# Optimization experiments

Hardware: AMD Instinct MI355X
Metric: run time of the kernel (lower is better)

## Reference

```python
import jax, jax.numpy as jnp
import numpy as np

V, E, H, L, T, B = 50257, 1024, 16, 12, 128, 16
FF = 4 * E
STD = 0.02


def setup_inputs() -> dict:
    key = jax.random.key(0)
    ks = jax.random.split(key, 20)
    n = lambda k, shape: (jax.random.normal(k, shape, dtype=jnp.float32) * STD)
    inp = {
        'idx': jax.random.randint(ks[0], (B, T), 0, V, dtype=jnp.int64),
        'targets': jax.random.randint(ks[1], (B, T), 0, V, dtype=jnp.int64),
        'tok_emb': n(ks[2], (V, E)),
        'pos_emb': n(ks[3], (T, E)),
        'wq': n(ks[4], (L, E, E)),
        'wk': n(ks[5], (L, E, E)),
        'wv': n(ks[6], (L, E, E)),
        'w_proj': n(ks[7], (L, E, E)),
        'b_proj': jnp.zeros((L, E), jnp.float32),
        'ln1_g': jnp.ones((L, E), jnp.float32),
        'ln1_b': jnp.zeros((L, E), jnp.float32),
        'ln2_g': jnp.ones((L, E), jnp.float32),
        'ln2_b': jnp.zeros((L, E), jnp.float32),
        'w_fc1': n(ks[8], (L, E, FF)),
        'b_fc1': jnp.zeros((L, FF), jnp.float32),
        'w_fc2': n(ks[9], (L, FF, E)),
        'b_fc2': jnp.zeros((L, E), jnp.float32),
        'lnf_g': jnp.ones((E,), jnp.float32),
        'lnf_b': jnp.zeros((E,), jnp.float32),
        'w_head': n(ks[10], (E, V)),
        'b_head': jnp.zeros((V,), jnp.float32),
    }
    return inp


def _layernorm(x, g, b, eps=1e-5):
    m = x.mean(-1, keepdims=True)
    v = ((x - m) ** 2).mean(-1, keepdims=True)
    return (x - m) / jnp.sqrt(v + eps) * g + b


def _forward(idx, targets, tok_emb, pos_emb, wq, wk, wv, w_proj, b_proj,
             ln1_g, ln1_b, ln2_g, ln2_b, w_fc1, b_fc1, w_fc2, b_fc2,
             lnf_g, lnf_b, w_head, b_head):
    Bb, Tt = idx.shape
    x = tok_emb[idx] + pos_emb[:Tt]  # (B, T, E)
    causal = jnp.tril(jnp.ones((Tt, Tt), dtype=bool))
    scale = E ** (-0.5)  # NOTE: original scales by full n_embd, not head_size

    def block(x, p):
        (wq_l, wk_l, wv_l, wp_l, bp_l, g1, b1, g2, b2, wf1, bf1, wf2, bf2) = p
        h = _layernorm(x, g1, b1)
        q = (h @ wq_l).reshape(Bb, Tt, H, -1)
        k = (h @ wk_l).reshape(Bb, Tt, H, -1)
        v = (h @ wv_l).reshape(Bb, Tt, H, -1)
        sc = jnp.einsum('bthd,bshd->bhts', q, k) * scale
        sc = jnp.where(causal, sc, -jnp.inf)
        att = jax.nn.softmax(sc, axis=-1)
        o = jnp.einsum('bhts,bshd->bthd', att, v).reshape(Bb, Tt, E)
        x = x + o @ wp_l + bp_l
        h2 = _layernorm(x, g2, b2)
        x = x + jax.nn.relu(h2 @ wf1 + bf1) @ wf2 + bf2
        return x, None

    x, _ = jax.lax.scan(block, x, (wq, wk, wv, w_proj, b_proj, ln1_g, ln1_b,
                                   ln2_g, ln2_b, w_fc1, b_fc1, w_fc2, b_fc2))
    x = _layernorm(x, lnf_g, lnf_b)
    logits = x @ w_head + b_head  # (B, T, V)
    logp = jax.nn.log_softmax(logits, axis=-1)
    nll = -jnp.take_along_axis(logp.reshape(Bb * Tt, -1),
                               targets.reshape(-1, 1), axis=1)
    loss = nll.mean()
    return logits, loss


def reference(idx, targets, tok_emb, pos_emb, wq, wk, wv, w_proj, b_proj,
              ln1_g, ln1_b, ln2_g, ln2_b, w_fc1, b_fc1, w_fc2, b_fc2,
              lnf_g, lnf_b, w_head, b_head):
    return _forward(idx, targets, tok_emb, pos_emb, wq, wk, wv, w_proj, b_proj,
                    ln1_g, ln1_b, ln2_g, ln2_b, w_fc1, b_fc1, w_fc2, b_fc2,
                    lnf_g, lnf_b, w_head, b_head)
```

## Files before the change

kernel.cpp:

```cpp
#include <hip/hip_runtime.h>
#include <math.h>

typedef unsigned short u16;
typedef float f32x4 __attribute__((ext_vector_type(4)));
typedef short bf16x8 __attribute__((ext_vector_type(8)));
typedef unsigned short us4 __attribute__((ext_vector_type(4)));

#define DEVI __device__ __forceinline__

DEVI float bf2f(u16 u) { return __uint_as_float(((unsigned int)u) << 16); }
DEVI u16 f2bf(float f) {
    unsigned int u = __float_as_uint(f);
    u += 0x7fffu + ((u >> 16) & 1u);
    return (u16)(u >> 16);
}

__global__ __launch_bounds__(256) void k_embed(const int* __restrict__ idx,
                                               const float* __restrict__ te,
                                               const float* __restrict__ pe,
                                               float* __restrict__ x) {
    int m = blockIdx.x;
    int t = m & 127;
    int tok = idx[m];
    const f32x4* a = (const f32x4*)(te + (long)tok * 1024);
    const f32x4* p = (const f32x4*)(pe + (long)t * 1024);
    f32x4* o = (f32x4*)(x + (long)m * 1024);
    o[threadIdx.x] = a[threadIdx.x] + p[threadIdx.x];
}

__global__ __launch_bounds__(256) void k_ln(const float* __restrict__ x,
                                            const float* __restrict__ g,
                                            const float* __restrict__ b,
                                            u16* __restrict__ out) {
    __shared__ float red[8];
    int tid = threadIdx.x, lane = tid & 63, wid = tid >> 6;
    int r = blockIdx.x;
    f32x4 v = ((const f32x4*)(x + (long)r * 1024))[tid];
    float s = v.x + v.y + v.z + v.w;
#pragma unroll
    for (int o2 = 32; o2; o2 >>= 1) s += __shfl_xor(s, o2);
    if (lane == 0) red[wid] = s;
    __syncthreads();
    float mean = (red[0] + red[1] + red[2] + red[3]) * (1.0f / 1024.0f);
    f32x4 d; d.x = v.x - mean; d.y = v.y - mean; d.z = v.z - mean; d.w = v.w - mean;
    float sq = d.x * d.x + d.y * d.y + d.z * d.z + d.w * d.w;
#pragma unroll
    for (int o2 = 32; o2; o2 >>= 1) sq += __shfl_xor(sq, o2);
    if (lane == 0) red[4 + wid] = sq;
    __syncthreads();
    float rstd = rsqrtf((red[4] + red[5] + red[6] + red[7]) * (1.0f / 1024.0f) + 1e-5f);
    f32x4 gg = ((const f32x4*)g)[tid];
    f32x4 bb = ((const f32x4*)b)[tid];
    us4 o4;
    o4.x = f2bf(d.x * rstd * gg.x + bb.x);
    o4.y = f2bf(d.y * rstd * gg.y + bb.y);
    o4.z = f2bf(d.z * rstd * gg.z + bb.z);
    o4.w = f2bf(d.w * rstd * gg.w + bb.w);
    ((us4*)(out + (long)r * 1024))[tid] = o4;
}

DEVI void tr_tile(const float* __restrict__ in, u16* __restrict__ out,
                  int K, int N, int k0, int n0, int tid, float (*tile)[65]) {
    int trow = tid >> 4;
    int tcol = (tid & 15) * 4;
#pragma unroll
    for (int p = 0; p < 4; ++p) {
        int k = k0 + trow + p * 16;
        const float* src = in + (long)k * N + n0 + tcol;
#pragma unroll
        for (int j = 0; j < 4; ++j) {
            int n = n0 + tcol + j;
            tile[trow + p * 16][tcol + j] = (n < N) ? src[j] : 0.0f;
        }
    }
    __syncthreads();
#pragma unroll
    for (int p = 0; p < 4; ++p) {
        int n = n0 + trow + p * 16;
        if (n < N) {
            us4 o4;
#pragma unroll
            for (int j = 0; j < 4; ++j) o4[j] = f2bf(tile[tcol + j][trow + p * 16]);
            *(us4*)(out + (long)n * K + k0 + tcol) = o4;
        }
    }
}

__global__ __launch_bounds__(256) void k_tr_one(const float* __restrict__ in,
                                                u16* __restrict__ out, int K, int N) {
    __shared__ float tile[64][65];
    tr_tile(in, out, K, N, blockIdx.y * 64, blockIdx.x * 64, threadIdx.x, tile);
}

__global__ __launch_bounds__(256) void k_tr_layer(
    const float* __restrict__ wq, const float* __restrict__ wk,
    const float* __restrict__ wv, const float* __restrict__ wp,
    const float* __restrict__ f1, const float* __restrict__ f2,
    u16* __restrict__ oqkv, u16* __restrict__ oproj,
    u16* __restrict__ of1, u16* __restrict__ of2) {
    __shared__ float tile[64][65];
    int id = blockIdx.x;
    const float* in; u16* out; int K, N, txx, tyy;
    if (id < 1024) {
        int t = id >> 8, s2 = id & 255;
        txx = s2 & 15; tyy = s2 >> 4; K = 1024; N = 1024;
        in = (t == 0) ? wq : (t == 1) ? wk : (t == 2) ? wv : wp;
        out = (t == 3) ? oproj : oqkv + (long)t * 1024 * 1024;
    } else if (id < 2048) {
        int s2 = id - 1024;
        txx = s2 & 63; tyy = s2 >> 6; K = 1024; N = 4096; in = f1; out = of1;
    } else {
        int s2 = id - 2048;
        txx = s2 & 15; tyy = s2 >> 4; K = 4096; N = 1024; in = f2; out = of2;
    }
    tr_tile(in, out, K, N, tyy * 64, txx * 64, threadIdx.x, tile);
}

template <int ROWS>
DEVI void stage_tile(const u16* __restrict__ g, long row0, long rowmax, int ld,
                     int col0, char* lds, int tid) {
    constexpr int NCH = ROWS * 8;
#pragma unroll
    for (int p = 0; p < NCH / 256; ++p) {
        int c = tid + p * 256;
        int row = c >> 3;
        int gslot = c & 7;
        int gdata = gslot ^ (row & 7);
        long gr = row0 + row;
        if (gr > rowmax) gr = rowmax;
        const u16* src = g + gr * (long)ld + col0 + gdata * 8;
        char* dst = lds + ((long)((tid & 192) + p * 256)) * 16;
        __builtin_amdgcn_global_load_lds(
            (const __attribute__((address_space(1))) void*)src,
            (__attribute__((address_space(3))) void*)dst, 16, 0, 0);
    }
}

template <int BN, bool OUT_BF16, bool RELU, bool HAS_BIAS, bool HAS_RES, bool GS, bool LP>
__global__ __launch_bounds__(256, 2) void k_gemm(
    const u16* __restrict__ A, const u16* __restrict__ Bt,
    const float* __restrict__ bias, const float* __restrict__ res,
    float* __restrict__ Cf, u16* __restrict__ Cb,
    int M, int N, int K, int ldc, float2* __restrict__ part, int ncb) {
    constexpr int NR = BN / 32;
    constexpr int ASZ = 128 * 64 * 2;
    constexpr int BSZ = BN * 64 * 2;
    __shared__ __align__(16) char lds[2 * (ASZ + BSZ)];
    int tid = threadIdx.x, lane = tid & 63, wid = tid >> 6;
    int l15 = lane & 15, l4 = lane >> 4;
    int wr = wid >> 1, wc = wid & 1;
    int bm = GS ? blockIdx.x : blockIdx.y;
    int bn = GS ? blockIdx.y : blockIdx.x;
    long m0 = (long)bm * 128;
    long n0 = (long)bn * BN;
    f32x4 acc[4][NR] = {};
    const int nk = K >> 6;

    stage_tile<128>(A, m0, (long)M - 1, K, 0, lds, tid);
    stage_tile<BN>(Bt, n0, (long)N - 1, K, 0, lds + ASZ, tid);
    int cur = 0;
    for (int kt = 0; kt < nk; ++kt) {
        __syncthreads();
        if (kt + 1 < nk) {
            char* nb = lds + (cur ^ 1) * (ASZ + BSZ);
            stage_tile<128>(A, m0, (long)M - 1, K, (kt + 1) << 6, nb, tid);
            stage_tile<BN>(Bt, n0, (long)N - 1, K, (kt + 1) << 6, nb + ASZ, tid);
        }
        const char* ab = lds + cur * (ASZ + BSZ);
        const char* bb = ab + ASZ;
#pragma unroll
        for (int kh = 0; kh < 2; ++kh) {
            bf16x8 af[4], bfv[NR];
#pragma unroll
            for (int mi = 0; mi < 4; ++mi) {
                int row = wr * 64 + mi * 16 + l15;
                int slot = (kh * 4 + l4) ^ (row & 7);
                af[mi] = *(const bf16x8*)(ab + (row * 8 + slot) * 16);
            }
#pragma unroll
            for (int ni = 0; ni < NR; ++ni) {
                int row = wc * (BN / 2) + ni * 16 + l15;
                int slot = (kh * 4 + l4) ^ (row & 7);
                bfv[ni] = *(const bf16x8*)(bb + (row * 8 + slot) * 16);
            }
#pragma unroll
            for (int mi = 0; mi < 4; ++mi)
#pragma unroll
                for (int ni = 0; ni < NR; ++ni)
                    acc[mi][ni] = __builtin_amdgcn_mfma_f32_16x16x32_bf16(
                        af[mi], bfv[ni], acc[mi][ni], 0, 0, 0);
        }
        cur ^= 1;
    }
    if constexpr (LP) {
        __shared__ float pmx[2][128], psm[2][128];
        float bvv[NR];
#pragma unroll
        for (int ni = 0; ni < NR; ++ni) {
            long n = n0 + wc * (BN / 2) + ni * 16 + l15;
            bvv[ni] = (HAS_BIAS && n < N) ? bias[n] : 0.0f;
        }
#pragma unroll
        for (int mi = 0; mi < 4; ++mi) {
#pragma unroll
            for (int j = 0; j < 4; ++j) {
                long m = m0 + wr * 64 + mi * 16 + l4 * 4 + j;
                float vv[NR];
                float mx = -INFINITY;
#pragma unroll
                for (int ni = 0; ni < NR; ++ni) {
                    long n = n0 + wc * (BN / 2) + ni * 16 + l15;
                    float v = acc[mi][ni][j] + bvv[ni];
                    if (n < N) Cf[m * (long)ldc + n] = v;
                    else v = -INFINITY;
                    vv[ni] = v;
                    mx = fmaxf(mx, v);
                }
#pragma unroll
                for (int ofs = 1; ofs < 16; ofs <<= 1) mx = fmaxf(mx, __shfl_xor(mx, ofs));
                float sm = 0.f;
#pragma unroll
                for (int ni = 0; ni < NR; ++ni) sm += __expf(vv[ni] - mx);
#pragma unroll
                for (int ofs = 1; ofs < 16; ofs <<= 1) sm += __shfl_xor(sm, ofs);
                if (l15 == 0) {
                    int r2 = wr * 64 + mi * 16 + l4 * 4 + j;
                    pmx[wc][r2] = mx;
                    psm[wc][r2] = sm;
                }
            }
        }
        __syncthreads();
        if (tid < 128) {
            float m1 = pmx[0][tid], m2 = pmx[1][tid];
            float nm = fmaxf(m1, m2);
            float S = psm[0][tid] * __expf(m1 - nm) + psm[1][tid] * __expf(m2 - nm);
            part[(m0 + tid) * (long)ncb + bn] = make_float2(nm, S);
        }
    } else {
#pragma unroll
        for (int ni = 0; ni < NR; ++ni) {
            long n = n0 + wc * (BN / 2) + ni * 16 + l15;
            if (n < N) {
                float bv = HAS_BIAS ? bias[n] : 0.0f;
#pragma unroll
                for (int mi = 0; mi < 4; ++mi) {
#pragma unroll
                    for (int j = 0; j < 4; ++j) {
                        long m = m0 + wr * 64 + mi * 16 + l4 * 4 + j;
                        float v = acc[mi][ni][j] + bv;
                        if (HAS_RES) v += res[m * (long)ldc + n];
                        if (RELU) v = fmaxf(v, 0.0f);
                        if (OUT_BF16) Cb[m * (long)ldc + n] = f2bf(v);
                        else Cf[m * (long)ldc + n] = v;
                    }
                }
            }
        }
    }
}

__global__ __launch_bounds__(256) void k_attn_mfma(const u16* __restrict__ qkv,
                                                   u16* __restrict__ o) {
    __shared__ __align__(16) u16 Ks[128 * 64];
    __shared__ __align__(16) u16 Vt[64 * 128];
    __shared__ __align__(16) u16 Ps[4][32 * 128];
    int tid = threadIdx.x, lane = tid & 63, w = tid >> 6;
    int l15 = lane & 15, l4 = lane >> 4;
    int b = blockIdx.x >> 4, h = blockIdx.x & 15;
    const u16* base = qkv + (long)b * 128 * 3072 + h * 64;

    stage_tile<128>(base + 1024, 0, 127, 3072, 0, (char*)Ks, tid);

    {
        const u16* vg = base + 2048;
#pragma unroll
        for (int p = 0; p < 4; ++p) {
            int s0 = (w * 4 + p) * 8;
            u16 tmp[8];
#pragma unroll
            for (int j = 0; j < 8; ++j) tmp[j] = vg[(long)(s0 + j) * 3072 + lane];
            int slot = (s0 >> 3) ^ (lane & 7);
            *(bf16x8*)((char*)Vt + lane * 256 + slot * 16) = *(bf16x8*)tmp;
        }
    }
    bf16x8 aq[2][2];
#pragma unroll
    for (int mj = 0; mj < 2; ++mj)
#pragma unroll
        for (int kk = 0; kk < 2; ++kk)
            aq[mj][kk] = *(const bf16x8*)(base + (long)(w * 32 + mj * 16 + l15) * 3072 + kk * 32 + l4 * 8);
    __syncthreads();

    f32x4 sacc[2][8] = {};
#pragma unroll
    for (int sj = 0; sj < 8; ++sj) {
        bf16x8 bk[2];
#pragma unroll
        for (int kk = 0; kk < 2; ++kk) {
            int row = sj * 16 + l15;
            int slot = (kk * 4 + l4) ^ (row & 7);
            bk[kk] = *(const bf16x8*)((char*)Ks + (row * 8 + slot) * 16);
        }
#pragma unroll
        for (int mj = 0; mj < 2; ++mj) {
            sacc[mj][sj] = __builtin_amdgcn_mfma_f32_16x16x32_bf16(aq[mj][0], bk[0], sacc[mj][sj], 0, 0, 0);
            sacc[mj][sj] = __builtin_amdgcn_mfma_f32_16x16x32_bf16(aq[mj][1], bk[1], sacc[mj][sj], 0, 0, 0);
        }
    }
    const float scale = 0.03125f;
#pragma unroll
    for (int mj = 0; mj < 2; ++mj) {
#pragma unroll
        for (int j = 0; j < 4; ++j) {
            int tq = w * 32 + mj * 16 + l4 * 4 + j;
            float mx = -INFINITY;
#pragma unroll
            for (int sj = 0; sj < 8; ++sj) {
                int s = sj * 16 + l15;
                float v = (s <= tq) ? sacc[mj][sj][j] * scale : -INFINITY;
                sacc[mj][sj][j] = v;
                mx = fmaxf(mx, v);
            }
#pragma unroll
            for (int ofs = 1; ofs < 16; ofs <<= 1) mx = fmaxf(mx, __shfl_xor(mx, ofs));
            float sm = 0.f;
#pragma unroll
            for (int sj = 0; sj < 8; ++sj) {
                float e = __expf(sacc[mj][sj][j] - mx);
                sacc[mj][sj][j] = e;
                sm += e;
            }
#pragma unroll
            for (int ofs = 1; ofs < 16; ofs <<= 1) sm += __shfl_xor(sm, ofs);
            float inv = 1.0f / sm;
            int m2 = mj * 16 + l4 * 4 + j;
            u16* prow = Ps[w] + m2 * 128;
#pragma unroll
            for (int sj = 0; sj < 8; ++sj) {
                int s = sj * 16 + l15;
                int slot = (s >> 3) ^ (m2 & 7);
                prow[slot * 8 + (s & 7)] = f2bf(sacc[mj][sj][j] * inv);
            }
        }
    }
    f32x4 oacc[2][4] = {};
#pragma unroll
    for (int kk = 0; kk < 4; ++kk) {
        bf16x8 pa[2], bv[4];
#pragma unroll
        for (int mj = 0; mj < 2; ++mj) {
            int m2 = mj * 16 + l15;
            int slot = (kk * 4 + l4) ^ (m2 & 7);
            pa[mj] = *(const bf16x8*)((char*)(Ps[w]) + m2 * 256 + slot * 16);
        }
#pragma unroll
        for (int nb = 0; nb < 4; ++nb) {
            int d = nb * 16 + l15;
            int slot = (kk * 4 + l4) ^ (d & 7);
            bv[nb] = *(const bf16x8*)((char*)Vt + d * 256 + slot * 16);
        }
#pragma unroll
        for (int mj = 0; mj < 2; ++mj)
#pragma unroll
            for (int nb = 0; nb < 4; ++nb)
                oacc[mj][nb] = __builtin_amdgcn_mfma_f32_16x16x32_bf16(pa[mj], bv[nb], oacc[mj][nb], 0, 0, 0);
    }
#pragma unroll
    for (int mj = 0; mj < 2; ++mj)
#pragma unroll
        for (int nb = 0; nb < 4; ++nb) {
            int d = nb * 16 + l15;
#pragma unroll
            for (int j = 0; j < 4; ++j) {
                int tq = w * 32 + mj * 16 + l4 * 4 + j;
                o[((long)b * 128 + tq) * 1024 + h * 64 + d] = f2bf(oacc[mj][nb][j]);
            }
        }
}

__global__ __launch_bounds__(64) void k_loss_rows2(const float2* __restrict__ part,
                                                   const float* __restrict__ logits,
                                                   const int* __restrict__ tgt,
                                                   float* __restrict__ rowloss, int ncb) {
    int r = blockIdx.x, lane = threadIdx.x;
    float M = -INFINITY, S = 0.f;
    for (int cb = lane; cb < ncb; cb += 64) {
        float2 p = part[(long)r * ncb + cb];
        float nm = fmaxf(M, p.x);
        S = S * __expf(M - nm) + p.y * __expf(p.x - nm);
        M = nm;
    }
#pragma unroll
    for (int ofs = 32; ofs; ofs >>= 1) {
        float M2 = __shfl_xor(M, ofs), S2 = __shfl_xor(S, ofs);
        float nm = fmaxf(M, M2);
        S = S * __expf(M - nm) + S2 * __expf(M2 - nm);
        M = nm;
    }
    if (lane == 0)
        rowloss[r] = (M + logf(S)) - logits[(long)r * 50257 + tgt[r]];
}

__global__ __launch_bounds__(256) void k_loss_reduce(const float* __restrict__ rowloss,
                                                     float* __restrict__ out) {
    __shared__ float red[4];
    int tid = threadIdx.x, lane = tid & 63, wid = tid >> 6;
    float s = 0.f;
    for (int i = tid; i < 2048; i += 256) s += rowloss[i];
#pragma unroll
    for (int ofs = 32; ofs; ofs >>= 1) s += __shfl_xor(s, ofs);
    if (lane == 0) red[wid] = s;
    __syncthreads();
    if (tid == 0) out[0] = (red[0] + red[1] + red[2] + red[3]) * (1.0f / 2048.0f);
}

extern "C" void kernel_launch(void* const* d_in, const int* in_sizes, int n_in,
                              void* d_out, int out_size, void* d_ws, size_t ws_size,
                              hipStream_t stream) {
    (void)in_sizes; (void)n_in; (void)out_size; (void)ws_size;
    const int*   idx     = (const int*)d_in[0];
    const int*   targets = (const int*)d_in[1];
    const float* tok_emb = (const float*)d_in[2];
    const float* pos_emb = (const float*)d_in[3];
    const float* wq      = (const float*)d_in[4];
    const float* wk      = (const float*)d_in[5];
    const float* wv      = (const float*)d_in[6];
    const float* w_proj  = (const float*)d_in[7];
    const float* b_proj  = (const float*)d_in[8];
    const float* ln1_g   = (const float*)d_in[9];
    const float* ln1_b   = (const float*)d_in[10];
    const float* ln2_g   = (const float*)d_in[11];
    const float* ln2_b   = (const float*)d_in[12];
    const float* w_fc1   = (const float*)d_in[13];
    const float* b_fc1   = (const float*)d_in[14];
    const float* w_fc2   = (const float*)d_in[15];
    const float* b_fc2   = (const float*)d_in[16];
    const float* lnf_g   = (const float*)d_in[17];
    const float* lnf_b   = (const float*)d_in[18];
    const float* w_head  = (const float*)d_in[19];
    const float* b_head  = (const float*)d_in[20];
    float* out = (float*)d_out;

    char* w = (char*)d_ws;
    auto alloc = [&](size_t bytes) {
        char* p = w;
        w += (bytes + 255) & ~(size_t)255;
        return p;
    };
    u16*    wT_qkv  = (u16*)alloc(3072L * 1024 * 2);
    u16*    wT_proj = (u16*)alloc(1024L * 1024 * 2);
    u16*    wT_f1   = (u16*)alloc(4096L * 1024 * 2);
    u16*    wT_f2   = (u16*)alloc(1024L * 4096 * 2);
    u16*    wT_head = (u16*)alloc(50257L * 1024 * 2);
    float*  x       = (float*)alloc(2048L * 1024 * 4);
    u16*    h_bf    = (u16*)alloc(2048L * 1024 * 2);
    u16*    qkvb    = (u16*)alloc(2048L * 3072 * 2);
    u16*    o_bf    = (u16*)alloc(2048L * 1024 * 2);
    u16*    ff_bf   = (u16*)alloc(2048L * 4096 * 2);
    float2* part    = (float2*)alloc(2048L * 393 * 8);
    float*  rowloss = (float*)alloc(2048L * 4);

    k_embed<<<2048, 256, 0, stream>>>(idx, tok_emb, pos_emb, x);
    k_tr_one<<<dim3(786, 16), 256, 0, stream>>>(w_head, wT_head, 1024, 50257);

    for (int l = 0; l < 12; ++l) {
        k_tr_layer<<<3072, 256, 0, stream>>>(
            wq + (long)l * 1048576, wk + (long)l * 1048576,
            wv + (long)l * 1048576, w_proj + (long)l * 1048576,
            w_fc1 + (long)l * 4194304, w_fc2 + (long)l * 4194304,
            wT_qkv, wT_proj, wT_f1, wT_f2);
        k_ln<<<2048, 256, 0, stream>>>(x, ln1_g + l * 1024, ln1_b + l * 1024, h_bf);
        k_gemm<64, true, false, false, false, false, false><<<dim3(48, 16), 256, 0, stream>>>(
            h_bf, wT_qkv, nullptr, nullptr, nullptr, qkvb, 2048, 3072, 1024, 3072, nullptr, 0);
        k_attn_mfma<<<256, 256, 0, stream>>>(qkvb, o_bf);
        k_gemm<64, false, false, true, true, false, false><<<dim3(16, 16), 256, 0, stream>>>(
            o_bf, wT_proj, b_proj + l * 1024, x, x, nullptr, 2048, 1024, 1024, 1024, nullptr, 0);
        k_ln<<<2048, 256, 0, stream>>>(x, ln2_g + l * 1024, ln2_b + l * 1024, h_bf);
        k_gemm<128, true, true, true, false, false, false><<<dim3(32, 16), 256, 0, stream>>>(
            h_bf, wT_f1, b_fc1 + l * 4096, nullptr, nullptr, ff_bf, 2048, 4096, 1024, 4096, nullptr, 0);
        k_gemm<64, false, false, true, true, false, false><<<dim3(16, 16), 256, 0, stream>>>(
            ff_bf, wT_f2, b_fc2 + l * 1024, x, x, nullptr, 2048, 1024, 4096, 1024, nullptr, 0);
    }
    k_ln<<<2048, 256, 0, stream>>>(x, lnf_g, lnf_b, h_bf);
    k_gemm<128, false, false, true, false, true, true><<<dim3(16, 393), 256, 0, stream>>>(
        h_bf, wT_head, b_head, nullptr, out, nullptr, 2048, 50257, 1024, 50257, part, 393);
    k_loss_rows2<<<2048, 64, 0, stream>>>(part, out, targets, rowloss, 393);
    k_loss_reduce<<<1, 256, 0, stream>>>(rowloss, out + 102926336L);
}
```

Measured before the change: 2.184 ms.

## Add dedicated 256x256-tile 512-thread LM-head GEMM with fused partial softmax

Replaces the generic 128x128 LM-head GEMM with a dedicated kernel. It uses 256x256 output tiles, 8 waves, a two-deep prefetch with explicit vmcnt waits and raw barriers, and raised priority during the MFMA loop. The larger tile is meant to cut re-reads of A and B and give more MFMA work per loaded byte on the dominant vocab GEMM. The fused per-tile max/sum partials now cover 256 columns, which halves the partial buffer. In exchange the kernel needs much more LDS and more registers per block, which may lower occupancy, and the -inf sentinel is replaced by -1e30.

```diff
diff --git a/kernel.cpp b/kernel.cpp
--- a/kernel.cpp
+++ b/kernel.cpp
@@ -136,12 +136,32 @@
     }
 }
 
-template <int BN, bool OUT_BF16, bool RELU, bool HAS_BIAS, bool HAS_RES, bool GS, bool LP>
+template <int ROWS>
+DEVI void stage512(const u16* __restrict__ g, long row0, long rowmax, int ld,
+                   int col0, char* lds, int tid) {
+    constexpr int NP = ROWS * 8 / 512;
+#pragma unroll
+    for (int p = 0; p < NP; ++p) {
+        int c = tid + p * 512;
+        int row = c >> 3;
+        int gslot = c & 7;
+        int gdata = gslot ^ (row & 7);
+        long gr = row0 + row;
+        if (gr > rowmax) gr = rowmax;
+        const u16* src = g + gr * (long)ld + col0 + gdata * 8;
+        char* dst = lds + ((long)((tid & 448) + p * 512)) * 16;
+        __builtin_amdgcn_global_load_lds(
+            (const __attribute__((address_space(1))) void*)src,
+            (__attribute__((address_space(3))) void*)dst, 16, 0, 0);
+    }
+}
+
+template <int BN, bool OUT_BF16, bool RELU, bool HAS_BIAS, bool HAS_RES>
 __global__ __launch_bounds__(256, 2) void k_gemm(
     const u16* __restrict__ A, const u16* __restrict__ Bt,
     const float* __restrict__ bias, const float* __restrict__ res,
     float* __restrict__ Cf, u16* __restrict__ Cb,
-    int M, int N, int K, int ldc, float2* __restrict__ part, int ncb) {
+    int M, int N, int K, int ldc) {
     constexpr int NR = BN / 32;
     constexpr int ASZ = 128 * 64 * 2;
     constexpr int BSZ = BN * 64 * 2;
@@ -149,10 +169,8 @@
     int tid = threadIdx.x, lane = tid & 63, wid = tid >> 6;
     int l15 = lane & 15, l4 = lane >> 4;
     int wr = wid >> 1, wc = wid & 1;
-    int bm = GS ? blockIdx.x : blockIdx.y;
-    int bn = GS ? blockIdx.y : blockIdx.x;
-    long m0 = (long)bm * 128;
-    long n0 = (long)bn * BN;
+    long m0 = (long)blockIdx.y * 128;
+    long n0 = (long)blockIdx.x * BN;
     f32x4 acc[4][NR] = {};
     const int nk = K >> 6;
 
@@ -192,71 +210,128 @@
         }
         cur ^= 1;
     }
-    if constexpr (LP) {
-        __shared__ float pmx[2][128], psm[2][128];
-        float bvv[NR];
-#pragma unroll
-        for (int ni = 0; ni < NR; ++ni) {
-            long n = n0 + wc * (BN / 2) + ni * 16 + l15;
-            bvv[ni] = (HAS_BIAS && n < N) ? bias[n] : 0.0f;
-        }
-#pragma unroll
-        for (int mi = 0; mi < 4; ++mi) {
-#pragma unroll
-            for (int j = 0; j < 4; ++j) {
-                long m = m0 + wr * 64 + mi * 16 + l4 * 4 + j;
-                float vv[NR];
-                float mx = -INFINITY;
-#pragma unroll
-                for (int ni = 0; ni < NR; ++ni) {
-                    long n = n0 + wc * (BN / 2) + ni * 16 + l15;
-                    float v = acc[mi][ni][j] + bvv[ni];
-                    if (n < N) Cf[m * (long)ldc + n] = v;
-                    else v = -INFINITY;
-                    vv[ni] = v;
-                    mx = fmaxf(mx, v);
+#pragma unroll
+    for (int ni = 0; ni < NR; ++ni) {
+        long n = n0 + wc * (BN / 2) + ni * 16 + l15;
+        if (n < N) {
+            float bv = HAS_BIAS ? bias[n] : 0.0f;
+#pragma unroll
+            for (int mi = 0; mi < 4; ++mi) {
+#pragma unroll
+                for (int j = 0; j < 4; ++j) {
+                    long m = m0 + wr * 64 + mi * 16 + l4 * 4 + j;
+                    float v = acc[mi][ni][j] + bv;
+                    if (HAS_RES) v += res[m * (long)ldc + n];
+                    if (RELU) v = fmaxf(v, 0.0f);
+                    if (OUT_BF16) Cb[m * (long)ldc + n] = f2bf(v);
+                    else Cf[m * (long)ldc + n] = v;
                 }
-#pragma unroll
-                for (int ofs = 1; ofs < 16; ofs <<= 1) mx = fmaxf(mx, __shfl_xor(mx, ofs));
-                float sm = 0.f;
-#pragma unroll
-                for (int ni = 0; ni < NR; ++ni) sm += __expf(vv[ni] - mx);
-#pragma unroll
-                for (int ofs = 1; ofs < 16; ofs <<= 1) sm += __shfl_xor(sm, ofs);
-                if (l15 == 0) {
-                    int r2 = wr * 64 + mi * 16 + l4 * 4 + j;
-                    pmx[wc][r2] = mx;
-                    psm[wc][r2] = sm;
-                }
-            }
-        }
-        __syncthreads();
-        if (tid < 128) {
-            float m1 = pmx[0][tid], m2 = pmx[1][tid];
-            float nm = fmaxf(m1, m2);
-            float S = psm[0][tid] * __expf(m1 - nm) + psm[1][tid] * __expf(m2 - nm);
-            part[(m0 + tid) * (long)ncb + bn] = make_float2(nm, S);
-        }
-    } else {
-#pragma unroll
-        for (int ni = 0; ni < NR; ++ni) {
-            long n = n0 + wc * (BN / 2) + ni * 16 + l15;
-            if (n < N) {
-                float bv = HAS_BIAS ? bias[n] : 0.0f;
-#pragma unroll
-                for (int mi = 0; mi < 4; ++mi) {
-#pragma unroll
-                    for (int j = 0; j < 4; ++j) {
-                        long m = m0 + wr * 64 + mi * 16 + l4 * 4 + j;
-                        float v = acc[mi][ni][j] + bv;
-                        if (HAS_RES) v += res[m * (long)ldc + n];
-                        if (RELU) v = fmaxf(v, 0.0f);
-                        if (OUT_BF16) Cb[m * (long)ldc + n] = f2bf(v);
-                        else Cf[m * (long)ldc + n] = v;
-                    }
-                }
-            }
-        }
+            }
+        }
+    }
+}
+
+__global__ __launch_bounds__(512, 2) void k_gemm_head(
+    const u16* __restrict__ A, const u16* __restrict__ Bt,
+    const float* __restrict__ bias, float* __restrict__ Cf,
+    float2* __restrict__ part, int M, int N, int K, int ldc, int ncb) {
+    constexpr int TSZ = 256 * 64 * 2;
+    __shared__ __align__(16) char lds[4 * TSZ];
+    __shared__ float pmx[4][256], psm[4][256];
+    int tid = threadIdx.x, lane = tid & 63, wid = tid >> 6;
+    int l15 = lane & 15, l4 = lane >> 4;
+    int wr = wid >> 2, wc = wid & 3;
+    int bm = blockIdx.x & 7, bn = blockIdx.x >> 3;
+    long m0 = (long)bm * 256, n0 = (long)bn * 256;
+    const int nk = K >> 6;
+    f32x4 acc[8][4] = {};
+
+    stage512<256>(A, m0, (long)M - 1, K, 0, lds, tid);
+    stage512<256>(Bt, n0, (long)N - 1, K, 0, lds + TSZ, tid);
+    stage512<256>(A, m0, (long)M - 1, K, 64, lds + 2 * TSZ, tid);
+    stage512<256>(Bt, n0, (long)N - 1, K, 64, lds + 3 * TSZ, tid);
+
+    for (int t = 0; t < nk; ++t) {
+        if (t < nk - 1) asm volatile("s_waitcnt vmcnt(8)" ::: "memory");
+        else            asm volatile("s_waitcnt vmcnt(0)" ::: "memory");
+        __builtin_amdgcn_s_barrier();
+        const char* ab = lds + (t & 1) * 2 * TSZ;
+        const char* bb = ab + TSZ;
+#pragma unroll
+        for (int kh = 0; kh < 2; ++kh) {
+            bf16x8 af[8], bfv[4];
+#pragma unroll
+            for (int mi = 0; mi < 8; ++mi) {
+                int row = wr * 128 + mi * 16 + l15;
+                int slot = (kh * 4 + l4) ^ (row & 7);
+                af[mi] = *(const bf16x8*)(ab + (row * 8 + slot) * 16);
+            }
+#pragma unroll
+            for (int ni = 0; ni < 4; ++ni) {
+                int row = wc * 64 + ni * 16 + l15;
+                int slot = (kh * 4 + l4) ^ (row & 7);
+                bfv[ni] = *(const bf16x8*)(bb + (row * 8 + slot) * 16);
+            }
+            __builtin_amdgcn_s_setprio(1);
+#pragma unroll
+            for (int mi = 0; mi < 8; ++mi)
+#pragma unroll
+                for (int ni = 0; ni < 4; ++ni)
+                    acc[mi][ni] = __builtin_amdgcn_mfma_f32_16x16x32_bf16(
+                        af[mi], bfv[ni], acc[mi][ni], 0, 0, 0);
+            __builtin_amdgcn_s_setprio(0);
+        }
+        __builtin_amdgcn_s_barrier();
+        if (t + 2 < nk) {
+            char* na = lds + (t & 1) * 2 * TSZ;
+            stage512<256>(A, m0, (long)M - 1, K, (t + 2) << 6, na, tid);
+            stage512<256>(Bt, n0, (long)N - 1, K, (t + 2) << 6, na + TSZ, tid);
+        }
+    }
+    const float BIG_NEG = -1e30f;
+    float bvv[4];
+#pragma unroll
+    for (int ni = 0; ni < 4; ++ni) {
+        long n = n0 + wc * 64 + ni * 16 + l15;
+        bvv[ni] = (n < N) ? bias[n] : 0.0f;
+    }
+#pragma unroll
+    for (int mi = 0; mi < 8; ++mi) {
+#pragma unroll
+        for (int j = 0; j < 4; ++j) {
+            int rloc = wr * 128 + mi * 16 + l4 * 4 + j;
+            long m = m0 + rloc;
+            float mx = BIG_NEG, vv[4];
+#pragma unroll
+            for (int ni = 0; ni < 4; ++ni) {
+                long n = n0 + wc * 64 + ni * 16 + l15;
+                float v = acc[mi][ni][j] + bvv[ni];
+                if (n < N) Cf[m * (long)ldc + n] = v;
+                else v = BIG_NEG;
+                vv[ni] = v;
+                mx = fmaxf(mx, v);
+            }
+#pragma unroll
+            for (int ofs = 1; ofs < 16; ofs <<= 1) mx = fmaxf(mx, __shfl_xor(mx, ofs));
+            float sm = 0.f;
+#pragma unroll
+            for (int ni = 0; ni < 4; ++ni) sm += __expf(vv[ni] - mx);
+#pragma unroll
+            for (int ofs = 1; ofs < 16; ofs <<= 1) sm += __shfl_xor(sm, ofs);
+            if (l15 == 0) { pmx[wc][rloc] = mx; psm[wc][rloc] = sm; }
+        }
+    }
+    __syncthreads();
+    if (tid < 256) {
+        float Mv = pmx[0][tid], Sv = psm[0][tid];
+#pragma unroll
+        for (int q = 1; q < 4; ++q) {
+            float m2 = pmx[q][tid], s2 = psm[q][tid];
+            float nm = fmaxf(Mv, m2);
+            Sv = Sv * __expf(Mv - nm) + s2 * __expf(m2 - nm);
+            Mv = nm;
+        }
+        part[(m0 + tid) * (long)ncb + bn] = make_float2(Mv, Sv);
     }
 }
 
@@ -271,7 +346,6 @@
     const u16* base = qkv + (long)b * 128 * 3072 + h * 64;
 
     stage_tile<128>(base + 1024, 0, 127, 3072, 0, (char*)Ks, tid);
-
     {
         const u16* vg = base + 2048;
 #pragma unroll
@@ -384,7 +458,7 @@
                                                    const int* __restrict__ tgt,
                                                    float* __restrict__ rowloss, int ncb) {
     int r = blockIdx.x, lane = threadIdx.x;
-    float M = -INFINITY, S = 0.f;
+    float M = -1e30f, S = 0.f;
     for (int cb = lane; cb < ncb; cb += 64) {
         float2 p = part[(long)r * ncb + cb];
         float nm = fmaxf(M, p.x);
@@ -458,7 +532,7 @@
     u16*    qkvb    = (u16*)alloc(2048L * 3072 * 2);
     u16*    o_bf    = (u16*)alloc(2048L * 1024 * 2);
     u16*    ff_bf   = (u16*)alloc(2048L * 4096 * 2);
-    float2* part    = (float2*)alloc(2048L * 393 * 8);
+    float2* part    = (float2*)alloc(2048L * 197 * 8);
     float*  rowloss = (float*)alloc(2048L * 4);
 
     k_embed<<<2048, 256, 0, stream>>>(idx, tok_emb, pos_emb, x);
@@ -471,20 +545,20 @@
             w_fc1 + (long)l * 4194304, w_fc2 + (long)l * 4194304,
             wT_qkv, wT_proj, wT_f1, wT_f2);
         k_ln<<<2048, 256, 0, stream>>>(x, ln1_g + l * 1024, ln1_b + l * 1024, h_bf);
-        k_gemm<64, true, false, false, false, false, false><<<dim3(48, 16), 256, 0, stream>>>(
-            h_bf, wT_qkv, nullptr, nullptr, nullptr, qkvb, 2048, 3072, 1024, 3072, nullptr, 0);
+        k_gemm<64, true, false, false, false><<<dim3(48, 16), 256, 0, stream>>>(
+            h_bf, wT_qkv, nullptr, nullptr, nullptr, qkvb, 2048, 3072, 1024, 3072);
         k_attn_mfma<<<256, 256, 0, stream>>>(qkvb, o_bf);
-        k_gemm<64, false, false, true, true, false, false><<<dim3(16, 16), 256, 0, stream>>>(
-            o_bf, wT_proj, b_proj + l * 1024, x, x, nullptr, 2048, 1024, 1024, 1024, nullptr, 0);
+        k_gemm<64, false, false, true, true><<<dim3(16, 16), 256, 0, stream>>>(
+            o_bf, wT_proj, b_proj + l * 1024, x, x, nullptr, 2048, 1024, 1024, 1024);
         k_ln<<<2048, 256, 0, stream>>>(x, ln2_g + l * 1024, ln2_b + l * 1024, h_bf);
-        k_gemm<128, true, true, true, false, false, false><<<dim3(32, 16), 256, 0, stream>>>(
-            h_bf, wT_f1, b_fc1 + l * 4096, nullptr, nullptr, ff_bf, 2048, 4096, 1024, 4096, nullptr, 0);
-        k_gemm<64, false, false, true, true, false, false><<<dim3(16, 16), 256, 0, stream>>>(
-            ff_bf, wT_f2, b_fc2 + l * 1024, x, x, nullptr, 2048, 1024, 4096, 1024, nullptr, 0);
+        k_gemm<128, true, true, true, false><<<dim3(32, 16), 256, 0, stream>>>(
+            h_bf, wT_f1, b_fc1 + l * 4096, nullptr, nullptr, ff_bf, 2048, 4096, 1024, 4096);
+        k_gemm<64, false, false, true, true><<<dim3(16, 16), 256, 0, stream>>>(
+            ff_bf, wT_f2, b_fc2 + l * 1024, x, x, nullptr, 2048, 1024, 4096, 1024);
     }
     k_ln<<<2048, 256, 0, stream>>>(x, lnf_g, lnf_b, h_bf);
-    k_gemm<128, false, false, true, false, true, true><<<dim3(16, 393), 256, 0, stream>>>(
-        h_bf, wT_head, b_head, nullptr, out, nullptr, 2048, 50257, 1024, 50257, part, 393);
-    k_loss_rows2<<<2048, 64, 0, stream>>>(part, out, targets, rowloss, 393);
+    k_gemm_head<<<1576, 512, 0, stream>>>(h_bf, wT_head, b_head, out, part,
+                                          2048, 50257, 1024, 50257, 197);
+    k_loss_rows2<<<2048, 64, 0, stream>>>(part, out, targets, rowloss, 197);
     k_loss_reduce<<<1, 256, 0, stream>>>(rowloss, out + 102926336L);
 }
```

New measurement: 2.158 ms. Within noise of the previous version (-1.2%).
